# Optimization experiments

Measured on AMD Instinct MI355X. Metric: run time of the kernel, lower is better.

Reference implementation:

```python
import jax, jax.numpy as jnp
from jax import lax
import numpy as np

WIN = 9  # default window [9, 9] in the original module


def _box_sum(x, win):
    """Sum over a win x win window, stride 1, pad win//2 (same as conv2d with ones kernel).
    Implemented separably (two 1D convs) - mathematically identical to the 2D ones-kernel conv.
    x: [B, 1, H, W] float32.
    """
    pad = win // 2
    kh = jnp.ones((1, 1, win, 1), x.dtype)
    kw = jnp.ones((1, 1, 1, win), x.dtype)
    dn = lax.conv_dimension_numbers(x.shape, kh.shape, ('NCHW', 'OIHW', 'NCHW'))
    y = lax.conv_general_dilated(x, kh, (1, 1), [(pad, pad), (0, 0)], dimension_numbers=dn)
    return lax.conv_general_dilated(y, kw, (1, 1), [(0, 0), (pad, pad)], dimension_numbers=dn)


def setup_inputs() -> dict:
    key = jax.random.key(0)
    k1, k2 = jax.random.split(key)
    shape = (32, 1, 512, 512)
    predict = jax.random.uniform(k1, shape, dtype=jnp.float32)
    target = jax.random.uniform(k2, shape, dtype=jnp.float32)
    return {"predict": predict, "target": target}


def reference(predict, target):
    win = WIN
    win_size = jnp.asarray(win * win, jnp.float32)

    I, J = predict, target
    I_sum = _box_sum(I, win)
    J_sum = _box_sum(J, win)
    I2_sum = _box_sum(I * I, win)
    J2_sum = _box_sum(J * J, win)
    IJ_sum = _box_sum(I * J, win)

    u_I = I_sum / win_size
    u_J = J_sum / win_size

    cross = IJ_sum - u_J * I_sum - u_I * J_sum + u_I * u_J * win_size
    I_var = I2_sum - 2.0 * u_I * I_sum + u_I * u_I * win_size
    J_var = J2_sum - 2.0 * u_J * J_sum + u_J * u_J * win_size

    cc = cross * cross / (I_var * J_var + 1e-6)
    return -jnp.mean(cc) + 1.0
```

## Files before the change

### kernel.cpp

```cpp
#include <hip/hip_runtime.h>


#define W 512
#define H 512
#define BH 8
#define NBANDS (H / BH)
#define NT 128

__device__ __forceinline__ float4 ld4(const float* p) {
    return *reinterpret_cast<const float4*>(p);
}

__global__ __launch_bounds__(NT)
void ncc_main(const float* __restrict__ I, const float* __restrict__ J,
              float* __restrict__ partials) {
    const int blk  = blockIdx.x;
    const int b    = blk / NBANDS;
    const int band = blk % NBANDS;
    const int y0   = band * BH;
    const float* Ip = I + (size_t)b * (H * W);
    const float* Jp = J + (size_t)b * (H * W);
    const int tid = threadIdx.x;
    const int x0  = tid * 4;

    __shared__ float4 xch[2][5][NT + 2];
    if (tid < 4) {
        int p = tid & 1, s = (tid >> 1) * (NT + 1);
        #pragma unroll
        for (int q = 0; q < 5; ++q)
            xch[p][q][s] = make_float4(0.f, 0.f, 0.f, 0.f);
    }

    float v[5][4];
    #pragma unroll
    for (int q = 0; q < 5; ++q)
        #pragma unroll
        for (int c = 0; c < 4; ++c) v[q][c] = 0.f;

    auto vadd = [&](int row) {
        float4 a = ld4(Ip + row * W + x0);
        float4 bb = ld4(Jp + row * W + x0);
        float av[4] = {a.x, a.y, a.z, a.w};
        float bv[4] = {bb.x, bb.y, bb.z, bb.w};
        #pragma unroll
        for (int c = 0; c < 4; ++c) {
            v[0][c] += av[c];
            v[1][c] += bv[c];
            v[2][c] += av[c] * av[c];
            v[3][c] += bv[c] * bv[c];
            v[4][c] += av[c] * bv[c];
        }
    };
    auto vsub = [&](int row) {
        float4 a = ld4(Ip + row * W + x0);
        float4 bb = ld4(Jp + row * W + x0);
        float av[4] = {a.x, a.y, a.z, a.w};
        float bv[4] = {bb.x, bb.y, bb.z, bb.w};
        #pragma unroll
        for (int c = 0; c < 4; ++c) {
            v[0][c] -= av[c];
            v[1][c] -= bv[c];
            v[2][c] -= av[c] * av[c];
            v[3][c] -= bv[c] * bv[c];
            v[4][c] -= av[c] * bv[c];
        }
    };

    #pragma unroll
    for (int dr = -4; dr < 4; ++dr) {
        int r = y0 + dr;
        if (r >= 0) vadd(r);
    }

    float cc_acc = 0.f;
    const float inv81 = 1.f / 81.f;
    #pragma unroll
    for (int i = 0; i < BH; ++i) {
        const int y = y0 + i;
        const int p = i & 1;
        if (y + 4 < H) vadd(y + 4);

        float4 pre[5];
        #pragma unroll
        for (int q = 0; q < 5; ++q) {
            float4 pr;
            pr.x = v[q][0];
            pr.y = pr.x + v[q][1];
            pr.z = pr.y + v[q][2];
            pr.w = pr.z + v[q][3];
            pre[q] = pr;
            xch[p][q][tid + 1] = pr;
        }
        __syncthreads();

        float h[5][4];
        #pragma unroll
        for (int q = 0; q < 5; ++q) {
            float4 L = xch[p][q][tid];
            float4 R = xch[p][q][tid + 2];
            float base = L.w + pre[q].w;
            h[q][0] = base + R.x;
            h[q][1] = (base - L.x) + R.y;
            h[q][2] = (base - L.y) + R.z;
            h[q][3] = (base - L.z) + R.w;
        }

        #pragma unroll
        for (int c = 0; c < 4; ++c) {
            float Is = h[0][c], Js = h[1][c];
            float I2 = h[2][c], J2 = h[3][c], IJ = h[4][c];
            float cross = IJ - Is * Js * inv81;
            float Ivar  = I2 - Is * Is * inv81;
            float Jvar  = J2 - Js * Js * inv81;
            cc_acc += cross * cross * __builtin_amdgcn_rcpf(Ivar * Jvar + 1e-6f);
        }

        if (y - 4 >= 0) vsub(y - 4);
    }

    #pragma unroll
    for (int off = 32; off > 0; off >>= 1)
        cc_acc += __shfl_down(cc_acc, off, 64);
    __shared__ float wsum[NT / 64];
    if ((tid & 63) == 0) wsum[tid >> 6] = cc_acc;
    __syncthreads();
    if (tid == 0) partials[blockIdx.x] = wsum[0] + wsum[1];
}

__global__ __launch_bounds__(256)
void ncc_finish(const float* __restrict__ partials, float* __restrict__ out,
                int n, float inv_total) {
    float v = 0.f;
    for (int i = threadIdx.x; i < n; i += blockDim.x) v += partials[i];
    #pragma unroll
    for (int off = 32; off > 0; off >>= 1)
        v += __shfl_down(v, off, 64);
    __shared__ float wsum[4];
    if ((threadIdx.x & 63) == 0) wsum[threadIdx.x >> 6] = v;
    __syncthreads();
    if (threadIdx.x == 0) {
        float t = wsum[0] + wsum[1] + wsum[2] + wsum[3];
        out[0] = 1.0f - t * inv_total;
    }
}

extern "C" void kernel_launch(void* const* d_in, const int* in_sizes, int n_in,
                              void* d_out, int out_size, void* d_ws, size_t ws_size,
                              hipStream_t stream) {
    const float* I = (const float*)d_in[0];
    const float* J = (const float*)d_in[1];
    float* out = (float*)d_out;
    float* partials = (float*)d_ws;

    const int n = in_sizes[0];
    const int B = n / (H * W);
    const int nblocks = B * NBANDS;

    ncc_main<<<nblocks, NT, 0, stream>>>(I, J, partials);
    ncc_finish<<<1, 256, 0, stream>>>(partials, out, nblocks, 1.0f / (float)n);
}
```

Measured before the change: 128.4 us.

## Make each wavefront own a full-width band and drop LDS halo exchange

Each 64-lane wavefront now processes one 4-row band across the full 512-pixel width, with 8 outputs per lane. Horizontal window neighbours are obtained by loading overlapping halo columns directly from global memory instead of exchanging prefix sums through shared memory with __syncthreads. This removes the per-row block barrier and LDS traffic, and the horizontal box sum becomes a sliding sum in registers. The cost is twice the global loads per row, more vertical-halo re-reads with the smaller band height, and higher register pressure from 80 accumulators per lane, with occupancy requested via launch bounds.

```diff
diff --git a/kernel.cpp b/kernel.cpp
--- a/kernel.cpp
+++ b/kernel.cpp
@@ -3,66 +3,79 @@
 
 #define W 512
 #define H 512
-#define BH 8
+#define BH 4
 #define NBANDS (H / BH)
-#define NT 128
+#define NT 256
+#define WPB 4
 
 __device__ __forceinline__ float4 ld4(const float* p) {
     return *reinterpret_cast<const float4*>(p);
 }
 
-__global__ __launch_bounds__(NT)
+__global__ __launch_bounds__(NT, 3)
 void ncc_main(const float* __restrict__ I, const float* __restrict__ J,
               float* __restrict__ partials) {
-    const int blk  = blockIdx.x;
-    const int b    = blk / NBANDS;
-    const int band = blk % NBANDS;
+    const int lane = threadIdx.x & 63;
+    const int wid  = threadIdx.x >> 6;
+    const int g    = blockIdx.x * WPB + wid;
+    const int b    = g >> 7;
+    const int band = g & (NBANDS - 1);
     const int y0   = band * BH;
     const float* Ip = I + (size_t)b * (H * W);
     const float* Jp = J + (size_t)b * (H * W);
-    const int tid = threadIdx.x;
-    const int x0  = tid * 4;
+    const int x0 = lane * 8;
 
-    __shared__ float4 xch[2][5][NT + 2];
-    if (tid < 4) {
-        int p = tid & 1, s = (tid >> 1) * (NT + 1);
-        #pragma unroll
-        for (int q = 0; q < 5; ++q)
-            xch[p][q][s] = make_float4(0.f, 0.f, 0.f, 0.f);
-    }
-
-    float v[5][4];
+    float v[5][16];
     #pragma unroll
     for (int q = 0; q < 5; ++q)
         #pragma unroll
-        for (int c = 0; c < 4; ++c) v[q][c] = 0.f;
+        for (int k = 0; k < 16; ++k) v[q][k] = 0.f;
+
+    const float4 zz = make_float4(0.f, 0.f, 0.f, 0.f);
+
+    auto loadrow = [&](int row, float a[16], float bb[16]) {
+        const float* ip = Ip + row * W;
+        const float* jp = Jp + row * W;
+        float4 A0 = (lane > 0)  ? ld4(ip + x0 - 4) : zz;
+        float4 A1 =               ld4(ip + x0);
+        float4 A2 =               ld4(ip + x0 + 4);
+        float4 A3 = (lane < 63) ? ld4(ip + x0 + 8) : zz;
+        float4 B0 = (lane > 0)  ? ld4(jp + x0 - 4) : zz;
+        float4 B1 =               ld4(jp + x0);
+        float4 B2 =               ld4(jp + x0 + 4);
+        float4 B3 = (lane < 63) ? ld4(jp + x0 + 8) : zz;
+        a[0]=A0.x; a[1]=A0.y; a[2]=A0.z; a[3]=A0.w;
+        a[4]=A1.x; a[5]=A1.y; a[6]=A1.z; a[7]=A1.w;
+        a[8]=A2.x; a[9]=A2.y; a[10]=A2.z; a[11]=A2.w;
+        a[12]=A3.x; a[13]=A3.y; a[14]=A3.z; a[15]=A3.w;
+        bb[0]=B0.x; bb[1]=B0.y; bb[2]=B0.z; bb[3]=B0.w;
+        bb[4]=B1.x; bb[5]=B1.y; bb[6]=B1.z; bb[7]=B1.w;
+        bb[8]=B2.x; bb[9]=B2.y; bb[10]=B2.z; bb[11]=B2.w;
+        bb[12]=B3.x; bb[13]=B3.y; bb[14]=B3.z; bb[15]=B3.w;
+    };
 
     auto vadd = [&](int row) {
-        float4 a = ld4(Ip + row * W + x0);
-        float4 bb = ld4(Jp + row * W + x0);
-        float av[4] = {a.x, a.y, a.z, a.w};
-        float bv[4] = {bb.x, bb.y, bb.z, bb.w};
+        float a[16], bb[16];
+        loadrow(row, a, bb);
         #pragma unroll
-        for (int c = 0; c < 4; ++c) {
-            v[0][c] += av[c];
-            v[1][c] += bv[c];
-            v[2][c] += av[c] * av[c];
-            v[3][c] += bv[c] * bv[c];
-            v[4][c] += av[c] * bv[c];
+        for (int k = 0; k < 16; ++k) {
+            v[0][k] += a[k];
+            v[1][k] += bb[k];
+            v[2][k] += a[k] * a[k];
+            v[3][k] += bb[k] * bb[k];
+            v[4][k] += a[k] * bb[k];
         }
     };
     auto vsub = [&](int row) {
-        float4 a = ld4(Ip + row * W + x0);
-        float4 bb = ld4(Jp + row * W + x0);
-        float av[4] = {a.x, a.y, a.z, a.w};
-        float bv[4] = {bb.x, bb.y, bb.z, bb.w};
+        float a[16], bb[16];
+        loadrow(row, a, bb);
         #pragma unroll
-        for (int c = 0; c < 4; ++c) {
-            v[0][c] -= av[c];
-            v[1][c] -= bv[c];
-            v[2][c] -= av[c] * av[c];
-            v[3][c] -= bv[c] * bv[c];
-            v[4][c] -= av[c] * bv[c];
+        for (int k = 0; k < 16; ++k) {
+            v[0][k] -= a[k];
+            v[1][k] -= bb[k];
+            v[2][k] -= a[k] * a[k];
+            v[3][k] -= bb[k] * bb[k];
+            v[4][k] -= a[k] * bb[k];
         }
     };
 
@@ -77,42 +90,32 @@
     #pragma unroll
     for (int i = 0; i < BH; ++i) {
         const int y = y0 + i;
-        const int p = i & 1;
         if (y + 4 < H) vadd(y + 4);
 
-        float4 pre[5];
+        float h[5][8];
         #pragma unroll
         for (int q = 0; q < 5; ++q) {
-            float4 pr;
-            pr.x = v[q][0];
-            pr.y = pr.x + v[q][1];
-            pr.z = pr.y + v[q][2];
-            pr.w = pr.z + v[q][3];
-            pre[q] = pr;
-            xch[p][q][tid + 1] = pr;
-        }
-        __syncthreads();
-
-        float h[5][4];
-        #pragma unroll
-        for (int q = 0; q < 5; ++q) {
-            float4 L = xch[p][q][tid];
-            float4 R = xch[p][q][tid + 2];
-            float base = L.w + pre[q].w;
-            h[q][0] = base + R.x;
-            h[q][1] = (base - L.x) + R.y;
-            h[q][2] = (base - L.y) + R.z;
-            h[q][3] = (base - L.z) + R.w;
+            float s01 = v[q][0] + v[q][1], s23 = v[q][2] + v[q][3];
+            float s45 = v[q][4] + v[q][5], s67 = v[q][6] + v[q][7];
+            float t = ((s01 + s23) + (s45 + s67)) + v[q][8];
+            h[q][0] = t;
+            #pragma unroll
+            for (int c = 1; c < 8; ++c) {
+                t += v[q][c + 8] - v[q][c - 1];
+                h[q][c] = t;
+            }
         }
 
         #pragma unroll
-        for (int c = 0; c < 4; ++c) {
+        for (int c = 0; c < 8; ++c) {
             float Is = h[0][c], Js = h[1][c];
             float I2 = h[2][c], J2 = h[3][c], IJ = h[4][c];
-            float cross = IJ - Is * Js * inv81;
-            float Ivar  = I2 - Is * Is * inv81;
-            float Jvar  = J2 - Js * Js * inv81;
-            cc_acc += cross * cross * __builtin_amdgcn_rcpf(Ivar * Jvar + 1e-6f);
+            float u     = Is * inv81;
+            float cross = IJ - u * Js;
+            float Ivar  = I2 - u * Is;
+            float Jvar  = J2 - (Js * inv81) * Js;
+            float r     = __builtin_amdgcn_rcpf(Ivar * Jvar + 1e-6f);
+            cc_acc += (cross * cross) * r;
         }
 
         if (y - 4 >= 0) vsub(y - 4);
@@ -121,10 +124,11 @@
     #pragma unroll
     for (int off = 32; off > 0; off >>= 1)
         cc_acc += __shfl_down(cc_acc, off, 64);
-    __shared__ float wsum[NT / 64];
-    if ((tid & 63) == 0) wsum[tid >> 6] = cc_acc;
+    __shared__ float wsum[WPB];
+    if (lane == 0) wsum[wid] = cc_acc;
     __syncthreads();
-    if (tid == 0) partials[blockIdx.x] = wsum[0] + wsum[1];
+    if (threadIdx.x == 0)
+        partials[blockIdx.x] = (wsum[0] + wsum[1]) + (wsum[2] + wsum[3]);
 }
 
 __global__ __launch_bounds__(256)
@@ -139,7 +143,7 @@
     if ((threadIdx.x & 63) == 0) wsum[threadIdx.x >> 6] = v;
     __syncthreads();
     if (threadIdx.x == 0) {
-        float t = wsum[0] + wsum[1] + wsum[2] + wsum[3];
+        float t = (wsum[0] + wsum[1]) + (wsum[2] + wsum[3]);
         out[0] = 1.0f - t * inv_total;
     }
 }
@@ -154,7 +158,7 @@
 
     const int n = in_sizes[0];
     const int B = n / (H * W);
-    const int nblocks = B * NBANDS;
+    const int nblocks = B * NBANDS / WPB;
 
     ncc_main<<<nblocks, NT, 0, stream>>>(I, J, partials);
     ncc_finish<<<1, 256, 0, stream>>>(partials, out, nblocks, 1.0f / (float)n);
```

After: 280.5 us. 118% more time.
